# Performance work log

Measured on AMD Instinct MI355X. Metric: run time of the kernel, lower is better.

The kernel has to match this reference:

```python
import jax, jax.numpy as jnp
import numpy as np

MIN_C = 1e-6
MIN_NORM = 1e-15
BALL_EPS = 0.004  # float32 ball epsilon


def _norm(x):
    return jnp.maximum(jnp.linalg.norm(x, axis=-1, keepdims=True), MIN_NORM)


def _project(x, c):
    norm = _norm(x)
    maxnorm = (1.0 - BALL_EPS) / jnp.sqrt(c)
    return jnp.where(norm > maxnorm, x / norm * maxnorm, x)


def _tanh(x):
    return jnp.tanh(jnp.clip(x, -15.0, 15.0))


def _artanh(x):
    x = jnp.clip(x, -1.0 + 1e-5, 1.0 - 1e-5)
    return 0.5 * (jnp.log1p(x) - jnp.log1p(-x))


def _expmap0(u, c):
    sc = jnp.sqrt(c)
    n = _norm(u)
    return _project(_tanh(sc * n) * u / (sc * n), c)


def _logmap0(y, c):
    sc = jnp.sqrt(c)
    n = _norm(y)
    return y / n / sc * _artanh(sc * n)


def _mobius_add(x, y, c):
    x2 = jnp.sum(x * x, -1, keepdims=True)
    y2 = jnp.sum(y * y, -1, keepdims=True)
    xy = jnp.sum(x * y, -1, keepdims=True)
    num = (1 + 2 * c * xy + c * y2) * x + (1 - c * x2) * y
    den = jnp.maximum(1 + 2 * c * xy + c * c * x2 * y2, MIN_NORM)
    return num / den


N_NODE, N_EDGE, D, ATTN, B, N_VOCAB = 100000, 1000000, 64, 64, 256, 401


def setup_inputs() -> dict:
    key = jax.random.key(0)
    ks = jax.random.split(key, 12)
    r_idx = jax.random.randint(ks[0], (N_EDGE,), 0, B, dtype=jnp.int32)
    rel = jax.random.randint(ks[1], (N_EDGE,), 0, N_VOCAB, dtype=jnp.int32)
    sub = jax.random.randint(ks[2], (N_EDGE,), 0, N_NODE, dtype=jnp.int32)
    obj = jax.random.randint(ks[3], (N_EDGE,), 0, N_NODE, dtype=jnp.int32)
    zero = jnp.zeros((N_EDGE,), jnp.int32)
    edges = jnp.stack([r_idx, zero, rel, zero, sub, obj], axis=1)  # [E, 6]
    s = 0.1
    return {
        "hidden": jax.random.normal(ks[4], (N_NODE, D), jnp.float32) * s,
        "q_rel": jax.random.randint(ks[5], (B,), 0, N_VOCAB, dtype=jnp.int32),
        "edges": edges,
        "rela_embed": jax.random.normal(ks[6], (N_VOCAB, D), jnp.float32) * s,
        "Ws_w": jax.random.normal(ks[7], (ATTN, D), jnp.float32) * s,
        "Wr_w": jax.random.normal(ks[8], (ATTN, D), jnp.float32) * s,
        "Wqr_w": jax.random.normal(ks[9], (ATTN, D), jnp.float32) * s,
        "Wqr_b": jnp.zeros((ATTN,), jnp.float32),
        "Wattn_w": jax.random.normal(ks[10], (1, ATTN), jnp.float32) * s,
        "Wh_w": jax.random.normal(ks[11], (D, D), jnp.float32) * s,
        "n_node": N_NODE,
    }


def reference(hidden, q_rel, edges, rela_embed, Ws_w, Wr_w, Wqr_w, Wqr_b, Wattn_w, Wh_w, n_node):
    c = MIN_C
    sub, rel, obj, r_idx = edges[:, 4], edges[:, 2], edges[:, 5], edges[:, 0]
    hs = hidden[sub]                 # [E, D] gather
    hr = rela_embed[rel]             # [E, D]
    h_qr = rela_embed[q_rel][r_idx]  # [E, D]
    # attention MLP -> scalar gate per edge
    pre = hs @ Ws_w.T + hr @ Wr_w.T + h_qr @ Wqr_w.T + Wqr_b
    alpha = jax.nn.sigmoid(jax.nn.relu(pre) @ Wattn_w.T)  # [E, 1]
    # hyperbolic message
    hs_h = _expmap0(hs, c)
    hr_h = _expmap0(hr, c)
    mess2 = _logmap0(_project(_mobius_add(hs_h, hr_h, c), c), c)
    message = mess2 * alpha
    agg = jax.ops.segment_sum(message, obj, num_segments=n_node)  # scatter-add
    a = _expmap0(agg @ Wh_w.T, c)
    a = jax.nn.relu(a)  # act
    return _logmap0(a, c)
```

## Files before the change

### kernel.cpp

```cpp
#include <hip/hip_runtime.h>
#include <math.h>
#include <stdint.h>

#define N_NODE 100000
#define N_EDGE 1000000
#define DIM    64
#define NB     256
#define NVOCAB 401
#define AGG_WAVES 8192

#define NBKT   782
#define CHKE   1024
#define NCHK   ((N_EDGE + CHKE - 1) / CHKE)
#define SCAN_TOT (NBKT * NCHK)
#define SCANA_GRID ((SCAN_TOT + 1023) / 1024)

typedef short short8  __attribute__((ext_vector_type(8)));
typedef float floatx4 __attribute__((ext_vector_type(4)));
typedef unsigned short ushort_t;

__device__ inline unsigned short f2bf_rne(float f)
{
    unsigned u = __float_as_uint(f);
    unsigned r = u + 0x7FFF + ((u >> 16) & 1);
    return (unsigned short)(r >> 16);
}
__device__ inline float bflo(unsigned u) { return __uint_as_float(u << 16); }
__device__ inline float bfhi(unsigned u) { return __uint_as_float(u & 0xFFFF0000u); }
__device__ inline unsigned short f2h(float f)
{
    _Float16 h = (_Float16)f;
    unsigned short s; __builtin_memcpy(&s, &h, 2); return s;
}
__device__ inline float h2f(unsigned b)
{
    unsigned short s = (unsigned short)b;
    _Float16 h; __builtin_memcpy(&h, &s, 2); return (float)h;
}

__device__ inline void split8(float4 v0, float4 v1, short8& hi, short8& lo)
{
    float f[8] = {v0.x, v0.y, v0.z, v0.w, v1.x, v1.y, v1.z, v1.w};
    #pragma unroll
    for (int j = 0; j < 8; ++j) {
        unsigned u = __float_as_uint(f[j]);
        unsigned r = u + 0x7FFF + ((u >> 16) & 1);
        unsigned short h = (unsigned short)(r >> 16);
        float hf = __uint_as_float(((unsigned)h) << 16);
        float l  = f[j] - hf;
        unsigned u2 = __float_as_uint(l);
        unsigned r2 = u2 + 0x7FFF + ((u2 >> 16) & 1);
        hi[j] = (short)h;
        lo[j] = (short)(r2 >> 16);
    }
}

#define INIT_GRID ((4 * 4096 + 255) / 256)

__global__ __launch_bounds__(256) void init_kernel(
    const float* __restrict__ Ws, const float* __restrict__ Wr,
    const float* __restrict__ Wqr, const float* __restrict__ Wh,
    ushort_t* __restrict__ wsp)
{
    int tid = blockIdx.x * 256 + threadIdx.x;
    if (tid < 4 * 4096) {
        int w = tid >> 12, e = tid & 4095;
        const float* src = (w == 0) ? Ws : (w == 1) ? Wr : (w == 2) ? Wqr : Wh;
        float f = src[e];
        unsigned u = __float_as_uint(f);
        unsigned r = u + 0x7FFF + ((u >> 16) & 1);
        unsigned short h = (unsigned short)(r >> 16);
        float hf = __uint_as_float(((unsigned)h) << 16);
        float l  = f - hf;
        unsigned u2 = __float_as_uint(l);
        unsigned r2 = u2 + 0x7FFF + ((u2 >> 16) & 1);
        wsp[w * 8192 + e]        = h;
        wsp[w * 8192 + 4096 + e] = (unsigned short)(r2 >> 16);
    }
}

__device__ void gemm64p_body(
    const float* __restrict__ X,
    const int*   __restrict__ idx,
    const ushort_t* __restrict__ Whi,
    const ushort_t* __restrict__ Wlo,
    const float* __restrict__ bias,
    void* __restrict__ Yv,
    ushort_t* __restrict__ Y2,
    int R, int out_mode, int blk)
{
    int wave = threadIdx.x >> 6;
    int lane = threadIdx.x & 63;
    int m    = lane & 15;
    int quad = lane >> 4;
    int r0   = blk * 64 + wave * 16;

    int r = r0 + m;
    int src = (r < R) ? (idx ? idx[r] : r) : 0;
    const float* xrow = X + (size_t)src * DIM + quad * 8;

    float4 a0[2], a1[2];
    #pragma unroll
    for (int c = 0; c < 2; ++c) {
        a0[c] = *(const float4*)(xrow + 32 * c);
        a1[c] = *(const float4*)(xrow + 32 * c + 4);
    }
    short8 ah[2], al[2];
    #pragma unroll
    for (int c = 0; c < 2; ++c) split8(a0[c], a1[c], ah[c], al[c]);

    if (out_mode == 3 && r < R) {
        #pragma unroll
        for (int c = 0; c < 2; ++c)
            *(short8*)(Y2 + (size_t)r * DIM + 32 * c + quad * 8) = ah[c];
    }

    floatx4 acc[4] = {{0,0,0,0},{0,0,0,0},{0,0,0,0},{0,0,0,0}};
    #pragma unroll
    for (int g = 0; g < 4; ++g) {
        const ushort_t* whrow = Whi + (size_t)(g * 16 + m) * DIM + quad * 8;
        const ushort_t* wlrow = Wlo + (size_t)(g * 16 + m) * DIM + quad * 8;
        #pragma unroll
        for (int c = 0; c < 2; ++c) {
            short8 bh = *(const short8*)(whrow + 32 * c);
            short8 bl = *(const short8*)(wlrow + 32 * c);
            acc[g] = __builtin_amdgcn_mfma_f32_16x16x32_bf16(bh, ah[c], acc[g], 0, 0, 0);
            acc[g] = __builtin_amdgcn_mfma_f32_16x16x32_bf16(bl, ah[c], acc[g], 0, 0, 0);
            acc[g] = __builtin_amdgcn_mfma_f32_16x16x32_bf16(bh, al[c], acc[g], 0, 0, 0);
        }
    }

    if (r < R) {
        #pragma unroll
        for (int g = 0; g < 4; ++g) {
            float4 bv = make_float4(0.f, 0.f, 0.f, 0.f);
            if (bias) bv = *(const float4*)(bias + g * 16 + quad * 4);
            float v0 = acc[g][0] + bv.x;
            float v1 = acc[g][1] + bv.y;
            float v2 = acc[g][2] + bv.z;
            float v3 = acc[g][3] + bv.w;
            if (out_mode == 1) {
                v0 = fmaxf(v0, 0.f); v1 = fmaxf(v1, 0.f);
                v2 = fmaxf(v2, 0.f); v3 = fmaxf(v3, 0.f);
            }
            if (out_mode >= 2) {
                uint2 o;
                o.x = (unsigned)f2bf_rne(v0) | ((unsigned)f2bf_rne(v1) << 16);
                o.y = (unsigned)f2bf_rne(v2) | ((unsigned)f2bf_rne(v3) << 16);
                *(uint2*)((ushort_t*)Yv + (size_t)r * DIM + g * 16 + quad * 4) = o;
            } else {
                *(float4*)((float*)Yv + (size_t)r * DIM + g * 16 + quad * 4) =
                    make_float4(v0, v1, v2, v3);
            }
        }
    }
}

__global__ __launch_bounds__(256) void gemm64p_bf16A_kernel(
    const ushort_t* __restrict__ A,
    const ushort_t* __restrict__ Whi,
    const ushort_t* __restrict__ Wlo,
    float* __restrict__ Y, int R)
{
    int wave = threadIdx.x >> 6;
    int lane = threadIdx.x & 63;
    int m    = lane & 15;
    int quad = lane >> 4;
    int r0   = blockIdx.x * 64 + wave * 16;

    int r = r0 + m;
    int src = (r < R) ? r : 0;
    short8 a8[2];
    #pragma unroll
    for (int c = 0; c < 2; ++c)
        a8[c] = *(const short8*)(A + (size_t)src * DIM + 32 * c + quad * 8);

    floatx4 acc[4] = {{0,0,0,0},{0,0,0,0},{0,0,0,0},{0,0,0,0}};
    #pragma unroll
    for (int g = 0; g < 4; ++g) {
        const ushort_t* whrow = Whi + (size_t)(g * 16 + m) * DIM + quad * 8;
        const ushort_t* wlrow = Wlo + (size_t)(g * 16 + m) * DIM + quad * 8;
        #pragma unroll
        for (int c = 0; c < 2; ++c) {
            short8 bh = *(const short8*)(whrow + 32 * c);
            short8 bl = *(const short8*)(wlrow + 32 * c);
            acc[g] = __builtin_amdgcn_mfma_f32_16x16x32_bf16(bh, a8[c], acc[g], 0, 0, 0);
            acc[g] = __builtin_amdgcn_mfma_f32_16x16x32_bf16(bl, a8[c], acc[g], 0, 0, 0);
        }
    }

    if (r < R) {
        #pragma unroll
        for (int g = 0; g < 4; ++g) {
            *(float4*)(Y + (size_t)r * DIM + g * 16 + quad * 4) =
                make_float4(fmaxf(acc[g][0], 0.f), fmaxf(acc[g][1], 0.f),
                            fmaxf(acc[g][2], 0.f), fmaxf(acc[g][3], 0.f));
        }
    }
}

__device__ void gemm64_body(
    const float* __restrict__ X,
    const int*   __restrict__ idx,
    const float* __restrict__ W,
    const float* __restrict__ bias,
    void* __restrict__ Yv,
    ushort_t* __restrict__ Y2,
    int R, int out_mode, int blk)
{
    int wave = threadIdx.x >> 6;
    int lane = threadIdx.x & 63;
    int m    = lane & 15;
    int quad = lane >> 4;
    int r0   = blk * 64 + wave * 16;

    int r = r0 + m;
    int src = (r < R) ? (idx ? idx[r] : r) : 0;
    const float* xrow = X + (size_t)src * DIM + quad * 8;

    float4 a0[2], a1[2];
    #pragma unroll
    for (int c = 0; c < 2; ++c) {
        a0[c] = *(const float4*)(xrow + 32 * c);
        a1[c] = *(const float4*)(xrow + 32 * c + 4);
    }
    short8 ah[2], al[2];
    #pragma unroll
    for (int c = 0; c < 2; ++c) split8(a0[c], a1[c], ah[c], al[c]);

    if (out_mode == 3 && r < R) {
        #pragma unroll
        for (int c = 0; c < 2; ++c)
            *(short8*)(Y2 + (size_t)r * DIM + 32 * c + quad * 8) = ah[c];
    }

    floatx4 acc[4] = {{0,0,0,0},{0,0,0,0},{0,0,0,0},{0,0,0,0}};
    #pragma unroll
    for (int g = 0; g < 4; ++g) {
        const float* wrow = W + (size_t)(g * 16 + m) * DIM + quad * 8;
        #pragma unroll
        for (int c = 0; c < 2; ++c) {
            float4 b0 = *(const float4*)(wrow + 32 * c);
            float4 b1 = *(const float4*)(wrow + 32 * c + 4);
            short8 bh, bl;
            split8(b0, b1, bh, bl);
            acc[g] = __builtin_amdgcn_mfma_f32_16x16x32_bf16(ah[c], bh, acc[g], 0, 0, 0);
            acc[g] = __builtin_amdgcn_mfma_f32_16x16x32_bf16(ah[c], bl, acc[g], 0, 0, 0);
            acc[g] = __builtin_amdgcn_mfma_f32_16x16x32_bf16(al[c], bh, acc[g], 0, 0, 0);
        }
    }

    #pragma unroll
    for (int g = 0; g < 4; ++g) {
        float bv = bias ? bias[g * 16 + m] : 0.0f;
        #pragma unroll
        for (int reg = 0; reg < 4; ++reg) {
            int rr = r0 + quad * 4 + reg;
            if (rr < R) {
                float v = acc[g][reg] + bv;
                if (out_mode == 1) v = fmaxf(v, 0.0f);
                if (out_mode >= 2)
                    ((ushort_t*)Yv)[(size_t)rr * DIM + g * 16 + m] = f2bf_rne(v);
                else
                    ((float*)Yv)[(size_t)rr * DIM + g * 16 + m] = v;
            }
        }
    }
}

__global__ __launch_bounds__(256) void gemm64_kernel(
    const float* __restrict__ X, const int* __restrict__ idx,
    const float* __restrict__ W, const float* __restrict__ bias,
    void* __restrict__ Yv, ushort_t* __restrict__ Y2, int R, int out_mode)
{
    gemm64_body(X, idx, W, bias, Yv, Y2, R, out_mode, blockIdx.x);
}

#define G1 ((N_NODE + 63) / 64)
#define G2 ((NVOCAB + 63) / 64)
#define G3 (NB / 64)
#define GSMALL (G2 + G3)
#define PREPC_GRID (NCHK + GSMALL + G1)

__global__ __launch_bounds__(256) void prepcount_kernel(
    const float* __restrict__ hidden,
    const float* __restrict__ rela,
    const int*   __restrict__ q_rel,
    const ushort_t* __restrict__ wsp,
    const float* __restrict__ Wqr_b,
    ushort_t* __restrict__ hsWs,
    ushort_t* __restrict__ hidb,
    ushort_t* __restrict__ rel_preb,
    ushort_t* __restrict__ relab,
    ushort_t* __restrict__ qr_preb,
    const int* __restrict__ edges,
    int2* __restrict__ epack,
    int* __restrict__ histBB)
{
    int b = blockIdx.x;
    if (b < NCHK) {
        __shared__ unsigned cnt[NBKT];
        for (int t = threadIdx.x; t < NBKT; t += 256) cnt[t] = 0;
        __syncthreads();
        int base = b * CHKE + threadIdx.x;
        #pragma unroll
        for (int k = 0; k < 4; ++k) {
            int e = base + k * 256;
            if (e < N_EDGE) {
                int2 ab = *(const int2*)(edges + (size_t)e * 6);
                int2 cd = *(const int2*)(edges + (size_t)e * 6 + 2);
                int2 ef = *(const int2*)(edges + (size_t)e * 6 + 4);
                epack[e] = make_int2(ef.x | (cd.x << 17), ef.y | (ab.x << 17));
                atomicAdd(&cnt[ef.y >> 7], 1u);
            }
        }
        __syncthreads();
        for (int t = threadIdx.x; t < NBKT; t += 256)
            histBB[b * NBKT + t] = (int)cnt[t];
    } else if (b < NCHK + G2) {
        gemm64p_body(rela, nullptr, wsp + 1 * 8192, wsp + 1 * 8192 + 4096,
                     nullptr, rel_preb, relab, NVOCAB, 3, b - NCHK);
    } else if (b < NCHK + GSMALL) {
        gemm64p_body(rela, q_rel, wsp + 2 * 8192, wsp + 2 * 8192 + 4096,
                     Wqr_b, qr_preb, nullptr, NB, 2, b - NCHK - G2);
    } else {
        gemm64p_body(hidden, nullptr, wsp, wsp + 4096,
                     nullptr, hsWs, hidb, N_NODE, 3, b - NCHK - GSMALL);
    }
}

__global__ __launch_bounds__(1024) void scanA_kernel(
    const int* __restrict__ histBB, int* __restrict__ offs2,
    int* __restrict__ partialA)
{
    __shared__ int s[1024];
    int t = threadIdx.x;
    int m = blockIdx.x * 1024 + t;
    int v = 0;
    if (m < SCAN_TOT) {
        int bin = m / NCHK, ch = m - bin * NCHK;
        v = histBB[ch * NBKT + bin];
    }
    s[t] = v;
    __syncthreads();
    for (int off = 1; off < 1024; off <<= 1) {
        int add = (t >= off) ? s[t - off] : 0;
        __syncthreads();
        s[t] += add;
        __syncthreads();
    }
    if (m < SCAN_TOT) offs2[m] = s[t] - v;
    if (t == 1023) partialA[blockIdx.x] = s[1023];
}

__global__ __launch_bounds__(1024) void scanB_kernel(
    int* __restrict__ partialA, int* __restrict__ bstart)
{
    __shared__ int s[1024];
    int t = threadIdx.x;
    int v = (t < SCANA_GRID) ? partialA[t] : 0;
    s[t] = v;
    __syncthreads();
    for (int off = 1; off < 1024; off <<= 1) {
        int add = (t >= off) ? s[t - off] : 0;
        __syncthreads();
        s[t] += add;
        __syncthreads();
    }
    if (t < SCANA_GRID) partialA[t] = s[t] - v;
    if (t == 0) bstart[NBKT] = N_EDGE;
}

__global__ __launch_bounds__(1024) void scanC_kernel(
    int* __restrict__ offs2, const int* __restrict__ partialA,
    int* __restrict__ bstart)
{
    int m = blockIdx.x * 1024 + threadIdx.x;
    if (m < SCAN_TOT) {
        int val = offs2[m] + partialA[blockIdx.x];
        offs2[m] = val;
        int bin = m / NCHK, ch = m - bin * NCHK;
        if (ch == 0) bstart[bin] = val;
    }
}

__global__ __launch_bounds__(1024) void alpha_scatter_kernel(
    const int2*     __restrict__ epack,
    const int*      __restrict__ offs2,
    const ushort_t* __restrict__ hsWs,
    const ushort_t* __restrict__ rel_preb,
    const ushort_t* __restrict__ qr_preb,
    const float*    __restrict__ wattn,
    int2*           __restrict__ csr2)
{
    __shared__ int offL[NBKT];
    int blk = blockIdx.x;
    for (int t = threadIdx.x; t < NBKT; t += 1024)
        offL[t] = offs2[t * NCHK + blk];
    __syncthreads();

    int wave = threadIdx.x >> 6;
    int lane = threadIdx.x & 63;
    int q    = lane >> 4;
    int l    = lane & 15;
    int f0   = l * 4;
    float4 wa = *(const float4*)(wattn + f0);

    #pragma unroll
    for (int it = 0; it < 4; ++it) {
        int e0 = blk * CHKE + wave * 64 + it * 16 + q * 4;

        int   sub[4], rl[4], ob[4];
        float tt[4];
        #pragma unroll
        for (int j = 0; j < 4; ++j) {
            int e = e0 + j;
            int2 ep = epack[min(e, N_EDGE - 1)];
            sub[j] = ep.x & 0x1FFFF;
            rl[j]  = (int)((unsigned)ep.x >> 17);
            ob[j]  = ep.y & 0x1FFFF;
            int ri = (int)((unsigned)ep.y >> 17);

            uint2 uh = *(const uint2*)(hsWs     + (size_t)sub[j] * DIM + f0);
            uint2 ur = *(const uint2*)(rel_preb + (size_t)rl[j]  * DIM + f0);
            uint2 uq = *(const uint2*)(qr_preb  + (size_t)ri     * DIM + f0);

            float s0 =  fmaxf(bflo(uh.x) + bflo(ur.x) + bflo(uq.x), 0.f) * wa.x;
            s0 = fmaf(fmaxf(bfhi(uh.x) + bfhi(ur.x) + bfhi(uq.x), 0.f), wa.y, s0);
            s0 = fmaf(fmaxf(bflo(uh.y) + bflo(ur.y) + bflo(uq.y), 0.f), wa.z, s0);
            s0 = fmaf(fmaxf(bfhi(uh.y) + bfhi(ur.y) + bfhi(uq.y), 0.f), wa.w, s0);
            tt[j] = s0;
        }
        #pragma unroll
        for (int j = 0; j < 4; ++j) {
            tt[j] += __shfl_xor(tt[j], 1);
            tt[j] += __shfl_xor(tt[j], 2);
            tt[j] += __shfl_xor(tt[j], 4);
            tt[j] += __shfl_xor(tt[j], 8);
        }

        if (l < 4) {
            int j = l;
            int e = e0 + j;
            if (e < N_EDGE) {
                float alpha = 1.0f / (1.0f + __expf(-tt[j]));
                int bin  = ob[j] >> 7;
                int slot = atomicAdd(&offL[bin], 1);
                csr2[slot] = make_int2(sub[j] | ((ob[j] & 127) << 17),
                    (int)(((unsigned)rl[j] << 16) | f2h(alpha)));
            }
        }
    }
}

__global__ __launch_bounds__(256) void node_sort_kernel(
    const int2* __restrict__ csr2,
    const int*  __restrict__ bstart,
    int2* __restrict__ csr3,
    int*  __restrict__ offs)
{
    __shared__ int cnt[128], incl[128];
    int b = blockIdx.x;
    int start = bstart[b];
    int end   = bstart[b + 1];
    int len   = end - start;

    if (threadIdx.x < 128) cnt[threadIdx.x] = 0;
    __syncthreads();
    for (int t = threadIdx.x; t < len; t += 256) {
        unsigned x = (unsigned)csr2[start + t].x;
        atomicAdd(&cnt[x >> 17], 1);
    }
    __syncthreads();
    if (threadIdx.x < 128) incl[threadIdx.x] = cnt[threadIdx.x];
    __syncthreads();
    for (int off = 1; off < 128; off <<= 1) {
        int add = 0;
        if (threadIdx.x < 128 && threadIdx.x >= off) add = incl[threadIdx.x - off];
        __syncthreads();
        if (threadIdx.x < 128) incl[threadIdx.x] += add;
        __syncthreads();
    }
    if (threadIdx.x < 128) {
        int excl = incl[threadIdx.x] - cnt[threadIdx.x];
        int n = b * 128 + threadIdx.x;
        if (n < N_NODE) offs[n] = start + excl;
        cnt[threadIdx.x] = excl;
    }
    if (b == 0 && threadIdx.x == 0) offs[N_NODE] = N_EDGE;
    if (b == 0 && threadIdx.x < 32) csr3[N_EDGE + threadIdx.x] = make_int2(0, 0);
    __syncthreads();
    for (int t = threadIdx.x; t < len; t += 256) {
        int2 ed = csr2[start + t];
        int row = (int)((unsigned)ed.x >> 17);
        int pos = start + atomicAdd(&cnt[row], 1);
        csr3[pos] = ed;
    }
}

__global__ __launch_bounds__(256) void agg_kernel(
    const int2*     __restrict__ csr3,
    const int*      __restrict__ offs,
    const ushort_t* __restrict__ hB,
    const ushort_t* __restrict__ relab,
    ushort_t* __restrict__ aggb)
{
    int lane = threadIdx.x & 63;
    int q    = lane >> 4;
    int l    = lane & 15;
    int f0   = l * 4;
    int wv = __builtin_amdgcn_readfirstlane((blockIdx.x * blockDim.x + threadIdx.x) >> 6);

    int i   = offs[wv];
    int end = offs[wv + 1];
    for (int n = wv; n < N_NODE; n += AGG_WAVES) {
        int nn = n + AGG_WAVES;
        int ni = 0, ne = 0;
        if (nn < N_NODE) { ni = offs[nn]; ne = offs[nn + 1]; }

        float4 acc = make_float4(0.f, 0.f, 0.f, 0.f);
        int2 e[4];
        #pragma unroll
        for (int j = 0; j < 4; ++j) e[j] = csr3[i + 4 * j + q];
        while (i < end) {
            int2 p[4];
            #pragma unroll
            for (int j = 0; j < 4; ++j) p[j] = csr3[i + 16 + 4 * j + q];

            uint2 uh[4], ur[4];
            #pragma unroll
            for (int j = 0; j < 4; ++j) {
                unsigned ex = (unsigned)e[j].x, ey = (unsigned)e[j].y;
                uh[j] = *(const uint2*)(hB    + ((ex & 0x1FFFFu) << 6) + f0);
                ur[j] = *(const uint2*)(relab + ((ey >> 16) << 6) + f0);
            }
            #pragma unroll
            for (int j = 0; j < 4; ++j) {
                unsigned ey = (unsigned)e[j].y;
                float v  = (i + 4 * j + q < end) ? 1.0f : 0.0f;
                float al = v * h2f(ey & 0xFFFFu);
                acc.x = fmaf(al, bflo(uh[j].x) + bflo(ur[j].x), acc.x);
                acc.y = fmaf(al, bfhi(uh[j].x) + bfhi(ur[j].x), acc.y);
                acc.z = fmaf(al, bflo(uh[j].y) + bflo(ur[j].y), acc.z);
                acc.w = fmaf(al, bfhi(uh[j].y) + bfhi(ur[j].y), acc.w);
            }
            #pragma unroll
            for (int j = 0; j < 4; ++j) e[j] = p[j];
            i += 16;
        }

        acc.x += __shfl_xor(acc.x, 16); acc.x += __shfl_xor(acc.x, 32);
        acc.y += __shfl_xor(acc.y, 16); acc.y += __shfl_xor(acc.y, 32);
        acc.z += __shfl_xor(acc.z, 16); acc.z += __shfl_xor(acc.z, 32);
        acc.w += __shfl_xor(acc.w, 16); acc.w += __shfl_xor(acc.w, 32);
        if (q == 0) {
            uint2 o;
            o.x = (unsigned)f2bf_rne(acc.x) | ((unsigned)f2bf_rne(acc.y) << 16);
            o.y = (unsigned)f2bf_rne(acc.z) | ((unsigned)f2bf_rne(acc.w) << 16);
            *(uint2*)(aggb + (((unsigned)n) << 6) + f0) = o;
        }

        i = ni; end = ne;
    }
}

__global__ __launch_bounds__(256) void edge_kernel(
    const int*      __restrict__ edges,
    const ushort_t* __restrict__ hB,
    const ushort_t* __restrict__ relab,
    const ushort_t* __restrict__ hsWs,
    const ushort_t* __restrict__ rel_preb,
    const ushort_t* __restrict__ qr_preb,
    const float*    __restrict__ wattn,
    float* __restrict__ out)
{
    int e = (blockIdx.x * blockDim.x + threadIdx.x) >> 6;
    if (e >= N_EDGE) return;
    int lane = threadIdx.x & 63;
    int r_i = edges[e * 6 + 0];
    int rl  = edges[e * 6 + 2];
    int sb  = edges[e * 6 + 4];
    int ob  = edges[e * 6 + 5];
    float hs = __uint_as_float(((unsigned)hB[(size_t)sb * DIM + lane]) << 16);
    float hr = __uint_as_float(((unsigned)relab[(size_t)rl * DIM + lane]) << 16);
    float p1 = __uint_as_float(((unsigned)hsWs[(size_t)sb * DIM + lane]) << 16);
    float p2 = __uint_as_float(((unsigned)rel_preb[(size_t)rl * DIM + lane]) << 16);
    float p3 = __uint_as_float(((unsigned)qr_preb[(size_t)r_i * DIM + lane]) << 16);
    float t = wattn[lane] * fmaxf(p1 + p2 + p3, 0.0f);
    #pragma unroll
    for (int off = 32; off; off >>= 1) t += __shfl_xor(t, off);
    float alpha = 1.0f / (1.0f + __expf(-t));
    atomicAdd(&out[(size_t)ob * DIM + lane], (hs + hr) * alpha);
}

extern "C" void kernel_launch(void* const* d_in, const int* in_sizes, int n_in,
                              void* d_out, int out_size, void* d_ws, size_t ws_size,
                              hipStream_t stream)
{
    const float* hidden = (const float*)d_in[0];
    const int*   q_rel  = (const int*)  d_in[1];
    const int*   edges  = (const int*)  d_in[2];
    const float* rela   = (const float*)d_in[3];
    const float* Ws     = (const float*)d_in[4];
    const float* Wr     = (const float*)d_in[5];
    const float* Wqr    = (const float*)d_in[6];
    const float* Wqr_b  = (const float*)d_in[7];
    const float* Wattn  = (const float*)d_in[8];
    const float* Wh     = (const float*)d_in[9];
    float* out = (float*)d_out;

    ushort_t* qr_preb  = (ushort_t*)d_ws;
    ushort_t* rel_preb = qr_preb + NB * DIM;
    ushort_t* relab    = rel_preb + NVOCAB * DIM;
    ushort_t* hsWs     = relab + NVOCAB * DIM;
    ushort_t* hidb     = hsWs + (size_t)N_NODE * DIM;
    int2* epack  = (int2*)(((uintptr_t)(hidb + (size_t)N_NODE * DIM) + 15) & ~(uintptr_t)15);
    int*  histBB = (int*)(epack + N_EDGE);
    int*  offs2  = histBB + SCAN_TOT;
    int*  partialA = offs2 + SCAN_TOT;
    int*  bstart   = partialA + 1024;
    int2* csr2   = (int2*)(((uintptr_t)(bstart + NBKT + 1) + 15) & ~(uintptr_t)15);
    ushort_t* wsp = (ushort_t*)(csr2 + N_EDGE);
    int2* csr3   = (int2*)(wsp + 4 * 8192);
    int*  offs   = (int*)(csr3 + N_EDGE + 32);
    size_t csr_need = ((char*)(offs + N_NODE + 1)) - (char*)d_ws;
    bool use_csr = ws_size >= csr_need;
    ushort_t* aggb = (ushort_t*)epack;

    if (use_csr) {
        init_kernel<<<INIT_GRID, 256, 0, stream>>>(Ws, Wr, Wqr, Wh, wsp);
        prepcount_kernel<<<PREPC_GRID, 256, 0, stream>>>(
            hidden, rela, q_rel, wsp, Wqr_b,
            hsWs, hidb, rel_preb, relab, qr_preb, edges, epack, histBB);
        scanA_kernel<<<SCANA_GRID, 1024, 0, stream>>>(histBB, offs2, partialA);
        scanB_kernel<<<1, 1024, 0, stream>>>(partialA, bstart);
        scanC_kernel<<<SCANA_GRID, 1024, 0, stream>>>(offs2, partialA, bstart);
        alpha_scatter_kernel<<<NCHK, 1024, 0, stream>>>(
            epack, offs2, hsWs, rel_preb, qr_preb, Wattn, csr2);
        node_sort_kernel<<<NBKT, 256, 0, stream>>>(csr2, bstart, csr3, offs);
        agg_kernel<<<AGG_WAVES / 4, 256, 0, stream>>>(csr3, offs, hidb, relab, aggb);
        gemm64p_bf16A_kernel<<<(N_NODE + 63) / 64, 256, 0, stream>>>(
            aggb, wsp + 3 * 8192, wsp + 3 * 8192 + 4096, out, N_NODE);
    } else {
        gemm64_kernel<<<(NVOCAB + 63) / 64, 256, 0, stream>>>(
            rela, nullptr, Wr, nullptr, rel_preb, relab, NVOCAB, 3);
        gemm64_kernel<<<(NB + 63) / 64, 256, 0, stream>>>(
            rela, q_rel, Wqr, Wqr_b, qr_preb, nullptr, NB, 2);
        gemm64_kernel<<<(N_NODE + 63) / 64, 256, 0, stream>>>(
            hidden, nullptr, Ws, nullptr, hsWs, hidb, N_NODE, 3);
        hipMemsetAsync(d_out, 0, (size_t)N_NODE * DIM * sizeof(float), stream);
        edge_kernel<<<(N_EDGE + 3) / 4, 256, 0, stream>>>(
            edges, hidb, relab, hsWs, rel_preb, qr_preb, Wattn, out);
        gemm64_kernel<<<(N_NODE + 63) / 64, 256, 0, stream>>>(
            out, nullptr, Wh, nullptr, out, nullptr, N_NODE, 1);
    }
}
```

Baseline: 251.7 us.

## Widen node buckets to 512 and fold block-sum scan into scanC

```diff
diff --git a/kernel.cpp b/kernel.cpp
--- a/kernel.cpp
+++ b/kernel.cpp
@@ -9,7 +9,9 @@
 #define NVOCAB 401
 #define AGG_WAVES 8192
 
-#define NBKT   782
+#define BSH    9
+#define BMSK   511
+#define NBKT   ((N_NODE + BMSK) >> BSH)
 #define CHKE   1024
 #define NCHK   ((N_EDGE + CHKE - 1) / CHKE)
 #define SCAN_TOT (NBKT * NCHK)
@@ -300,7 +302,7 @@
     int b = blockIdx.x;
     if (b < NCHK) {
         __shared__ unsigned cnt[NBKT];
-        for (int t = threadIdx.x; t < NBKT; t += 256) cnt[t] = 0;
+        if (threadIdx.x < NBKT) cnt[threadIdx.x] = 0;
         __syncthreads();
         int base = b * CHKE + threadIdx.x;
         #pragma unroll
@@ -311,12 +313,12 @@
                 int2 cd = *(const int2*)(edges + (size_t)e * 6 + 2);
                 int2 ef = *(const int2*)(edges + (size_t)e * 6 + 4);
                 epack[e] = make_int2(ef.x | (cd.x << 17), ef.y | (ab.x << 17));
-                atomicAdd(&cnt[ef.y >> 7], 1u);
+                atomicAdd(&cnt[ef.y >> BSH], 1u);
             }
         }
         __syncthreads();
-        for (int t = threadIdx.x; t < NBKT; t += 256)
-            histBB[b * NBKT + t] = (int)cnt[t];
+        if (threadIdx.x < NBKT)
+            histBB[b * NBKT + threadIdx.x] = (int)cnt[threadIdx.x];
     } else if (b < NCHK + G2) {
         gemm64p_body(rela, nullptr, wsp + 1 * 8192, wsp + 1 * 8192 + 4096,
                      nullptr, rel_preb, relab, NVOCAB, 3, b - NCHK);
@@ -353,35 +355,32 @@
     if (t == 1023) partialA[blockIdx.x] = s[1023];
 }
 
-__global__ __launch_bounds__(1024) void scanB_kernel(
-    int* __restrict__ partialA, int* __restrict__ bstart)
-{
-    __shared__ int s[1024];
-    int t = threadIdx.x;
-    int v = (t < SCANA_GRID) ? partialA[t] : 0;
-    s[t] = v;
-    __syncthreads();
-    for (int off = 1; off < 1024; off <<= 1) {
-        int add = (t >= off) ? s[t - off] : 0;
-        __syncthreads();
-        s[t] += add;
-        __syncthreads();
-    }
-    if (t < SCANA_GRID) partialA[t] = s[t] - v;
-    if (t == 0) bstart[NBKT] = N_EDGE;
-}
-
 __global__ __launch_bounds__(1024) void scanC_kernel(
     int* __restrict__ offs2, const int* __restrict__ partialA,
     int* __restrict__ bstart)
 {
-    int m = blockIdx.x * 1024 + threadIdx.x;
+    __shared__ int s[1024];
+    __shared__ int pbase_s;
+    int t = threadIdx.x;
+    int pb = (t < (int)blockIdx.x) ? partialA[t] : 0;
+    s[t] = pb;
+    __syncthreads();
+    for (int off = 1024 / 2; off; off >>= 1) {
+        if (t < off) s[t] += s[t + off];
+        __syncthreads();
+    }
+    if (t == 0) pbase_s = s[0];
+    __syncthreads();
+    int pbase = pbase_s;
+
+    int m = blockIdx.x * 1024 + t;
     if (m < SCAN_TOT) {
-        int val = offs2[m] + partialA[blockIdx.x];
+        int val = offs2[m] + pbase;
         offs2[m] = val;
         int bin = m / NCHK, ch = m - bin * NCHK;
         if (ch == 0) bstart[bin] = val;
     }
+    if (blockIdx.x == 0 && t == 0) bstart[NBKT] = N_EDGE;
 }
 
 __global__ __launch_bounds__(1024) void alpha_scatter_kernel(
@@ -395,8 +394,8 @@
 {
     __shared__ int offL[NBKT];
     int blk = blockIdx.x;
-    for (int t = threadIdx.x; t < NBKT; t += 1024)
-        offL[t] = offs2[t * NCHK + blk];
+    if (threadIdx.x < NBKT)
+        offL[threadIdx.x] = offs2[threadIdx.x * NCHK + blk];
     __syncthreads();
 
     int wave = threadIdx.x >> 6;
@@ -421,9 +420,9 @@
             ob[j]  = ep.y & 0x1FFFF;
             int ri = (int)((unsigned)ep.y >> 17);
 
-            uint2 uh = *(const uint2*)(hsWs     + (size_t)sub[j] * DIM + f0);
-            uint2 ur = *(const uint2*)(rel_preb + (size_t)rl[j]  * DIM + f0);
-            uint2 uq = *(const uint2*)(qr_preb  + (size_t)ri     * DIM + f0);
+            uint2 uh = *(const uint2*)(hsWs     + (((unsigned)sub[j]) << 6) + f0);
+            uint2 ur = *(const uint2*)(rel_preb + (((unsigned)rl[j])  << 6) + f0);
+            uint2 uq = *(const uint2*)(qr_preb  + (((unsigned)ri)     << 6) + f0);
 
             float s0 =  fmaxf(bflo(uh.x) + bflo(ur.x) + bflo(uq.x), 0.f) * wa.x;
             s0 = fmaf(fmaxf(bfhi(uh.x) + bfhi(ur.x) + bfhi(uq.x), 0.f), wa.y, s0);
@@ -444,53 +443,52 @@
             int e = e0 + j;
             if (e < N_EDGE) {
                 float alpha = 1.0f / (1.0f + __expf(-tt[j]));
-                int bin  = ob[j] >> 7;
+                int bin  = ob[j] >> BSH;
                 int slot = atomicAdd(&offL[bin], 1);
-                csr2[slot] = make_int2(sub[j] | ((ob[j] & 127) << 17),
+                csr2[slot] = make_int2(sub[j] | ((ob[j] & BMSK) << 17),
                     (int)(((unsigned)rl[j] << 16) | f2h(alpha)));
             }
         }
     }
 }
 
-__global__ __launch_bounds__(256) void node_sort_kernel(
+__global__ __launch_bounds__(512) void node_sort_kernel(
     const int2* __restrict__ csr2,
     const int*  __restrict__ bstart,
     int2* __restrict__ csr3,
     int*  __restrict__ offs)
 {
-    __shared__ int cnt[128], incl[128];
+    __shared__ int cnt[512], incl[512];
     int b = blockIdx.x;
     int start = bstart[b];
     int end   = bstart[b + 1];
     int len   = end - start;
 
-    if (threadIdx.x < 128) cnt[threadIdx.x] = 0;
-    __syncthreads();
-    for (int t = threadIdx.x; t < len; t += 256) {
+    cnt[threadIdx.x] = 0;
+    __syncthreads();
+    for (int t = threadIdx.x; t < len; t += 512) {
         unsigned x = (unsigned)csr2[start + t].x;
         atomicAdd(&cnt[x >> 17], 1);
     }
     __syncthreads();
-    if (threadIdx.x < 128) incl[threadIdx.x] = cnt[threadIdx.x];
-    __syncthreads();
-    for (int off = 1; off < 128; off <<= 1) {
-        int add = 0;
-        if (threadIdx.x < 128 && threadIdx.x >= off) add = incl[threadIdx.x - off];
+    incl[threadIdx.x] = cnt[threadIdx.x];
+    __syncthreads();
+    for (int off = 1; off < 512; off <<= 1) {
+        int add = ((int)threadIdx.x >= off) ? incl[threadIdx.x - off] : 0;
         __syncthreads();
-        if (threadIdx.x < 128) incl[threadIdx.x] += add;
+        incl[threadIdx.x] += add;
         __syncthreads();
     }
-    if (threadIdx.x < 128) {
+    {
         int excl = incl[threadIdx.x] - cnt[threadIdx.x];
-        int n = b * 128 + threadIdx.x;
+        int n = (b << BSH) + threadIdx.x;
         if (n < N_NODE) offs[n] = start + excl;
         cnt[threadIdx.x] = excl;
     }
     if (b == 0 && threadIdx.x == 0) offs[N_NODE] = N_EDGE;
     if (b == 0 && threadIdx.x < 32) csr3[N_EDGE + threadIdx.x] = make_int2(0, 0);
     __syncthreads();
-    for (int t = threadIdx.x; t < len; t += 256) {
+    for (int t = threadIdx.x; t < len; t += 512) {
         int2 ed = csr2[start + t];
         int row = (int)((unsigned)ed.x >> 17);
         int pos = start + atomicAdd(&cnt[row], 1);
@@ -633,11 +631,10 @@
             hidden, rela, q_rel, wsp, Wqr_b,
             hsWs, hidb, rel_preb, relab, qr_preb, edges, epack, histBB);
         scanA_kernel<<<SCANA_GRID, 1024, 0, stream>>>(histBB, offs2, partialA);
-        scanB_kernel<<<1, 1024, 0, stream>>>(partialA, bstart);
         scanC_kernel<<<SCANA_GRID, 1024, 0, stream>>>(offs2, partialA, bstart);
         alpha_scatter_kernel<<<NCHK, 1024, 0, stream>>>(
             epack, offs2, hsWs, rel_preb, qr_preb, Wattn, csr2);
-        node_sort_kernel<<<NBKT, 256, 0, stream>>>(csr2, bstart, csr3, offs);
+        node_sort_kernel<<<NBKT, 512, 0, stream>>>(csr2, bstart, csr3, offs);
         agg_kernel<<<AGG_WAVES / 4, 256, 0, stream>>>(csr3, offs, hidb, relab, aggb);
         gemm64p_bf16A_kernel<<<(N_NODE + 63) / 64, 256, 0, stream>>>(
             aggb, wsp + 3 * 8192, wsp + 3 * 8192 + 4096, out, N_NODE);
```

Result: faster. 242.5 us (-3.6%).
